# Performance work log

Measured on AMD Instinct MI355X. Metric: run time of the kernel, lower is better.

## Reference

```python
import jax, jax.numpy as jnp
import numpy as np

SEQ, B, IN, H = 1024, 1024, 64, 64

def setup_inputs() -> dict:
    key = jax.random.key(0)
    ks = jax.random.split(key, 6)
    s_in = 1.0 / np.sqrt(IN)
    s_h = 1.0 / np.sqrt(H)
    return {
        "x": jax.random.normal(ks[0], (SEQ, B, IN), dtype=jnp.float32),
        "h": jax.random.normal(ks[1], (1, B, H), dtype=jnp.float32),
        # nn.Linear params: weight (out,in), bias (out,)
        "Wx": jax.random.uniform(ks[2], (H, IN), jnp.float32, -s_in, s_in),
        "bx": jax.random.uniform(ks[3], (H,), jnp.float32, -s_in, s_in),
        "Wh": jax.random.uniform(ks[4], (H, H), jnp.float32, -s_h, s_h),
        "bh": jax.random.uniform(ks[5], (H,), jnp.float32, -s_h, s_h),
    }

def reference(x, h, Wx, bx, Wh, bh):
    act = jnp.tanh  # activation='tanh'
    # Precompute input projection for all timesteps: (S,B,H)
    xp = jnp.einsum('sbi,hi->sbh', x, Wx) + bx
    # lin_h(h).sum(0) with h of shape (1,B,H) == lin_h(h[0])
    h0 = act(jnp.einsum('bj,hj->bh', h[0], Wh) + bh + xp[0])

    def step(h_prev, xt):
        h_new = act(jnp.einsum('bj,hj->bh', h_prev, Wh) + bh + xt)
        return h_new, h_new

    h_last, h_rest = jax.lax.scan(step, h0, xp[1:])
    h_seq = jnp.concatenate([h0[None], h_rest], axis=0)  # (S,B,H)
    return h_seq, h_last
```

## Files before the change

### kernel.cpp

```cpp
#include <hip/hip_runtime.h>
#include <stdint.h>

#define SEQ 1024
#define NB  1024
#define HD  64
#define BH  (NB*HD)
#define ROWS_PER_BLK 8

typedef _Float16 f16x8 __attribute__((ext_vector_type(8)));
typedef float    f32x4 __attribute__((ext_vector_type(4)));

__device__ __forceinline__ int swzb(int s) {
    return (s * 16) ^ (((s >> 3) & 7) << 4);
}
__device__ __forceinline__ uint32_t pkrtz(float a, float b) {
    auto h = __builtin_amdgcn_cvt_pkrtz(a, b);
    return __builtin_bit_cast(uint32_t, h);
}
__device__ __forceinline__ float fast_tanh(float a) {
    float e = __builtin_amdgcn_exp2f(a * 2.8853900817779268f);
    return 1.0f - 2.0f * __builtin_amdgcn_rcpf(e + 1.0f);
}

__global__ __launch_bounds__(256) void rnn_kernel(
    const float* __restrict__ x,  const float* __restrict__ h0,
    const float* __restrict__ Wx, const float* __restrict__ bx,
    const float* __restrict__ Wh, const float* __restrict__ bh,
    float* __restrict__ out)
{
    __shared__ uint32_t lds[2][4][256];

    const int tid  = threadIdx.x;
    const int w    = tid >> 6;
    const int lane = tid & 63;
    const int g    = lane >> 4;
    const int n    = lane & 15;
    const int R0   = blockIdx.x * ROWS_PER_BLK;

    const int pT = tid >> 7;
    const int pr = tid & 127;
    const int pg = pr >> 5;
    const int pn = (pr >> 2) & 7;
    const int pq = pr & 3;
    const int k0 = pT * 32 + pg * 8 + pq * 2;
    const int pdw = (swzb(pg * 16 + pn) >> 2) + pq;
    const float* xprod = x + (size_t)(R0 + pn) * HD + k0;

    const int rdw = swzb(lane) >> 2;

    const int hTw = w >> 1;
    const int hdw = (swzb((2 * (w & 1) + (g >> 1)) * 16 + n) >> 2) + 2 * (g & 1);

    const int jrow = 16 * w + n;
    f16x8 whA[2], wxA[2];
    {
        const float* wr = Wh + (size_t)jrow * HD;
        const float* xr = Wx + (size_t)jrow * HD;
        #pragma unroll
        for (int T = 0; T < 2; ++T) {
            f16x8 aw, ax;
            #pragma unroll
            for (int e = 0; e < 8; ++e) {
                aw[e] = (_Float16)wr[T * 32 + g * 8 + e];
                ax[e] = (_Float16)xr[T * 32 + g * 8 + e];
            }
            whA[T] = aw; wxA[T] = ax;
        }
    }
    f32x4 bias;
    {
        const int j4 = 16 * w + 4 * g;
        #pragma unroll
        for (int r = 0; r < 4; ++r) bias[r] = bh[j4 + r] + bx[j4 + r];
    }

    {
        int4 z = {0, 0, 0, 0};
        ((int4*)lds)[tid]       = z;
        ((int4*)lds)[tid + 256] = z;
    }
    __syncthreads();

    {
        float2 hv = *(const float2*)(h0 + (size_t)(R0 + pn) * HD + k0);
        lds[0][pT][pdw] = pkrtz(hv.x, hv.y);
        float2 xv = *(const float2*)(xprod);
        lds[0][2 + pT][pdw] = pkrtz(xv.x, xv.y);
    }
    float2 r1 = *(const float2*)(xprod + (size_t)1 * BH);
    float2 r2 = *(const float2*)(xprod + (size_t)2 * BH);
    float2 r3 = *(const float2*)(xprod + (size_t)3 * BH);
    float2 r0 = *(const float2*)(xprod + (size_t)4 * BH);
    __syncthreads();

    f16x8 fh0, fh1, fx0, fx1;
    fh0 = __builtin_bit_cast(f16x8, *(const int4*)&lds[0][0][rdw]);
    fh1 = __builtin_bit_cast(f16x8, *(const int4*)&lds[0][1][rdw]);
    fx0 = __builtin_bit_cast(f16x8, *(const int4*)&lds[0][2][rdw]);
    fx1 = __builtin_bit_cast(f16x8, *(const int4*)&lds[0][3][rdw]);

    float* outlast = out + (size_t)SEQ * BH;

    auto STEP = [&](int t, float2& rn) {
        f32x4 acc;
        acc = __builtin_amdgcn_mfma_f32_16x16x32_f16(wxA[0], fx0, bias, 0, 0, 0);
        acc = __builtin_amdgcn_mfma_f32_16x16x32_f16(wxA[1], fx1, acc,  0, 0, 0);
        acc = __builtin_amdgcn_mfma_f32_16x16x32_f16(whA[0], fh0, acc,  0, 0, 0);
        acc = __builtin_amdgcn_mfma_f32_16x16x32_f16(whA[1], fh1, acc,  0, 0, 0);

        const int b2 = (t + 1) & 1;
        if (t < SEQ - 1) {
            lds[b2][2 + pT][pdw] = pkrtz(rn.x, rn.y);
        }
        {
            int tl = t + 5; if (tl > SEQ - 1) tl = SEQ - 1;
            rn = *(const float2*)(xprod + (size_t)tl * BH);
        }

        float hv0 = fast_tanh(acc[0]);
        float hv1 = fast_tanh(acc[1]);
        float hv2 = fast_tanh(acc[2]);
        float hv3 = fast_tanh(acc[3]);

        if (t < SEQ - 1) {
            uint32_t e0 = pkrtz(hv0, hv1);
            uint32_t e1 = pkrtz(hv2, hv3);
            *(int2*)&lds[b2][hTw][hdw] = make_int2((int)e0, (int)e1);
            __syncthreads();
            fh0 = __builtin_bit_cast(f16x8, *(const int4*)&lds[b2][0][rdw]);
            fh1 = __builtin_bit_cast(f16x8, *(const int4*)&lds[b2][1][rdw]);
            fx0 = __builtin_bit_cast(f16x8, *(const int4*)&lds[b2][2][rdw]);
            fx1 = __builtin_bit_cast(f16x8, *(const int4*)&lds[b2][3][rdw]);
        }
        if (n < 8) {
            float4 v = make_float4(hv0, hv1, hv2, hv3);
            float* dst = out + (size_t)t * BH + (size_t)(R0 + n) * HD + 16 * w + 4 * g;
            *(float4*)dst = v;
            if (t == SEQ - 1) {
                *(float4*)(outlast + (size_t)(R0 + n) * HD + 16 * w + 4 * g) = v;
            }
        }
    };

    for (int tb = 0; tb < SEQ; tb += 4) {
        STEP(tb + 0, r1);
        STEP(tb + 1, r2);
        STEP(tb + 2, r3);
        STEP(tb + 3, r0);
    }
}

extern "C" void kernel_launch(void* const* d_in, const int* in_sizes, int n_in,
                              void* d_out, int out_size, void* d_ws, size_t ws_size,
                              hipStream_t stream) {
    const float* x  = (const float*)d_in[0];
    const float* h  = (const float*)d_in[1];
    const float* Wx = (const float*)d_in[2];
    const float* bx = (const float*)d_in[3];
    const float* Wh = (const float*)d_in[4];
    const float* bh = (const float*)d_in[5];
    float* out = (float*)d_out;

    rnn_kernel<<<dim3(NB / ROWS_PER_BLK), dim3(256), 0, stream>>>(x, h, Wx, bx, Wh, bh, out);
}
```

Before: 295.7 us.

## Precompute next-step input projection off the recurrent critical path

The input-projection MFMAs for step t+1 now run during step t, using a 4-deep x ring buffer in LDS, so only two dependent Wh MFMAs remain on the serial chain. Those two are split into independent accumulators and summed, which shortens the MFMA dependency depth. A custom barrier waits only on LDS counters, and the global output store now sits before the barrier. The cost is extra LDS, a vector add, and a prefetch distance lengthened by one step.

```diff
diff --git a/kernel.cpp b/kernel.cpp
--- a/kernel.cpp
+++ b/kernel.cpp
@@ -21,6 +21,11 @@
     float e = __builtin_amdgcn_exp2f(a * 2.8853900817779268f);
     return 1.0f - 2.0f * __builtin_amdgcn_rcpf(e + 1.0f);
 }
+__device__ __forceinline__ void sync_lds() {
+    asm volatile("s_waitcnt lgkmcnt(0)" ::: "memory");
+    __builtin_amdgcn_s_barrier();
+    asm volatile("" ::: "memory");
+}
 
 __global__ __launch_bounds__(256) void rnn_kernel(
     const float* __restrict__ x,  const float* __restrict__ h0,
@@ -28,7 +33,8 @@
     const float* __restrict__ Wh, const float* __restrict__ bh,
     float* __restrict__ out)
 {
-    __shared__ uint32_t lds[2][4][256];
+    __shared__ __align__(16) uint32_t hK[2][2][256];
+    __shared__ __align__(16) uint32_t xK[4][2][256];
 
     const int tid  = threadIdx.x;
     const int w    = tid >> 6;
@@ -76,61 +82,63 @@
 
     {
         int4 z = {0, 0, 0, 0};
-        ((int4*)lds)[tid]       = z;
-        ((int4*)lds)[tid + 256] = z;
+        ((int4*)hK)[tid] = z;
+        ((int4*)xK)[tid] = z;
+        ((int4*)xK)[tid + 256] = z;
     }
-    __syncthreads();
+    sync_lds();
 
     {
         float2 hv = *(const float2*)(h0 + (size_t)(R0 + pn) * HD + k0);
-        lds[0][pT][pdw] = pkrtz(hv.x, hv.y);
-        float2 xv = *(const float2*)(xprod);
-        lds[0][2 + pT][pdw] = pkrtz(xv.x, xv.y);
+        hK[0][pT][pdw] = pkrtz(hv.x, hv.y);
+        float2 x0v = *(const float2*)(xprod);
+        xK[0][pT][pdw] = pkrtz(x0v.x, x0v.y);
+        float2 x1v = *(const float2*)(xprod + (size_t)BH);
+        xK[1][pT][pdw] = pkrtz(x1v.x, x1v.y);
     }
-    float2 r1 = *(const float2*)(xprod + (size_t)1 * BH);
-    float2 r2 = *(const float2*)(xprod + (size_t)2 * BH);
-    float2 r3 = *(const float2*)(xprod + (size_t)3 * BH);
-    float2 r0 = *(const float2*)(xprod + (size_t)4 * BH);
-    __syncthreads();
+    float2 r0 = *(const float2*)(xprod + (size_t)2 * BH);
+    float2 r1 = *(const float2*)(xprod + (size_t)3 * BH);
+    float2 r2 = *(const float2*)(xprod + (size_t)4 * BH);
+    float2 r3 = *(const float2*)(xprod + (size_t)5 * BH);
+    sync_lds();
 
-    f16x8 fh0, fh1, fx0, fx1;
-    fh0 = __builtin_bit_cast(f16x8, *(const int4*)&lds[0][0][rdw]);
-    fh1 = __builtin_bit_cast(f16x8, *(const int4*)&lds[0][1][rdw]);
-    fx0 = __builtin_bit_cast(f16x8, *(const int4*)&lds[0][2][rdw]);
-    fx1 = __builtin_bit_cast(f16x8, *(const int4*)&lds[0][3][rdw]);
-
+    f16x8 fh0 = __builtin_bit_cast(f16x8, *(const int4*)&hK[0][0][rdw]);
+    f16x8 fh1 = __builtin_bit_cast(f16x8, *(const int4*)&hK[0][1][rdw]);
+    const f32x4 zf = {0.f, 0.f, 0.f, 0.f};
+    f32x4 xpA, xpB;
+    {
+        f16x8 fx0 = __builtin_bit_cast(f16x8, *(const int4*)&xK[0][0][rdw]);
+        f16x8 fx1 = __builtin_bit_cast(f16x8, *(const int4*)&xK[0][1][rdw]);
+        xpA = __builtin_amdgcn_mfma_f32_16x16x32_f16(wxA[0], fx0, bias, 0, 0, 0);
+        xpB = __builtin_amdgcn_mfma_f32_16x16x32_f16(wxA[1], fx1, zf,   0, 0, 0);
+    }
     float* outlast = out + (size_t)SEQ * BH;
 
     auto STEP = [&](int t, float2& rn) {
-        f32x4 acc;
-        acc = __builtin_amdgcn_mfma_f32_16x16x32_f16(wxA[0], fx0, bias, 0, 0, 0);
-        acc = __builtin_amdgcn_mfma_f32_16x16x32_f16(wxA[1], fx1, acc,  0, 0, 0);
-        acc = __builtin_amdgcn_mfma_f32_16x16x32_f16(whA[0], fh0, acc,  0, 0, 0);
-        acc = __builtin_amdgcn_mfma_f32_16x16x32_f16(whA[1], fh1, acc,  0, 0, 0);
+        f32x4 accA = __builtin_amdgcn_mfma_f32_16x16x32_f16(whA[0], fh0, xpA, 0, 0, 0);
+        f32x4 accB = __builtin_amdgcn_mfma_f32_16x16x32_f16(whA[1], fh1, xpB, 0, 0, 0);
 
-        const int b2 = (t + 1) & 1;
-        if (t < SEQ - 1) {
-            lds[b2][2 + pT][pdw] = pkrtz(rn.x, rn.y);
-        }
+        if (t + 2 < SEQ) xK[(t + 2) & 3][pT][pdw] = pkrtz(rn.x, rn.y);
         {
-            int tl = t + 5; if (tl > SEQ - 1) tl = SEQ - 1;
+            int tl = t + 6; if (tl > SEQ - 1) tl = SEQ - 1;
             rn = *(const float2*)(xprod + (size_t)tl * BH);
         }
+        if (t + 1 < SEQ) {
+            f16x8 fxn0 = __builtin_bit_cast(f16x8, *(const int4*)&xK[(t + 1) & 3][0][rdw]);
+            f16x8 fxn1 = __builtin_bit_cast(f16x8, *(const int4*)&xK[(t + 1) & 3][1][rdw]);
+            xpA = __builtin_amdgcn_mfma_f32_16x16x32_f16(wxA[0], fxn0, bias, 0, 0, 0);
+            xpB = __builtin_amdgcn_mfma_f32_16x16x32_f16(wxA[1], fxn1, zf,   0, 0, 0);
+        }
 
+        f32x4 acc = accA + accB;
         float hv0 = fast_tanh(acc[0]);
         float hv1 = fast_tanh(acc[1]);
         float hv2 = fast_tanh(acc[2]);
         float hv3 = fast_tanh(acc[3]);
 
-        if (t < SEQ - 1) {
-            uint32_t e0 = pkrtz(hv0, hv1);
-            uint32_t e1 = pkrtz(hv2, hv3);
-            *(int2*)&lds[b2][hTw][hdw] = make_int2((int)e0, (int)e1);
-            __syncthreads();
-            fh0 = __builtin_bit_cast(f16x8, *(const int4*)&lds[b2][0][rdw]);
-            fh1 = __builtin_bit_cast(f16x8, *(const int4*)&lds[b2][1][rdw]);
-            fx0 = __builtin_bit_cast(f16x8, *(const int4*)&lds[b2][2][rdw]);
-            fx1 = __builtin_bit_cast(f16x8, *(const int4*)&lds[b2][3][rdw]);
+        if (t + 1 < SEQ) {
+            *(int2*)&hK[(t + 1) & 1][hTw][hdw] =
+                make_int2((int)pkrtz(hv0, hv1), (int)pkrtz(hv2, hv3));
         }
         if (n < 8) {
             float4 v = make_float4(hv0, hv1, hv2, hv3);
@@ -140,13 +148,18 @@
                 *(float4*)(outlast + (size_t)(R0 + n) * HD + 16 * w + 4 * g) = v;
             }
         }
+        if (t + 1 < SEQ) {
+            sync_lds();
+            fh0 = __builtin_bit_cast(f16x8, *(const int4*)&hK[(t + 1) & 1][0][rdw]);
+            fh1 = __builtin_bit_cast(f16x8, *(const int4*)&hK[(t + 1) & 1][1][rdw]);
+        }
     };
 
     for (int tb = 0; tb < SEQ; tb += 4) {
-        STEP(tb + 0, r1);
-        STEP(tb + 1, r2);
-        STEP(tb + 2, r3);
-        STEP(tb + 3, r0);
+        STEP(tb + 0, r0);
+        STEP(tb + 1, r1);
+        STEP(tb + 2, r2);
+        STEP(tb + 3, r3);
     }
 }
 
```

Result: slower. 308.4 us (+4.3%).

## Run each batch tile in one wavefront using cross-lane permutes instead of LDS barriers

Applied to the files above, without the earlier changes.

Each block now holds all four 16-row output tiles in a single 64-lane wavefront. The recurrent hidden state is redistributed between lanes with permlane32/16 swaps (falling back to ds_bpermute), which removes the per-step LDS write, __syncthreads and LDS reads. The input projection for the next step is computed by MFMA off the critical path, and log2(e)*2 is folded into the weights and bias so tanh needs no multiply. The cost is a 4x larger serial MFMA chain per wave, fewer waves overall, and a runtime probe of permlane semantics to pick the shuffle variant.

```diff
diff --git a/kernel.cpp b/kernel.cpp
--- a/kernel.cpp
+++ b/kernel.cpp
@@ -5,149 +5,232 @@
 #define NB  1024
 #define HD  64
 #define BH  (NB*HD)
-#define ROWS_PER_BLK 8
+#define RPW 8
 
 typedef _Float16 f16x8 __attribute__((ext_vector_type(8)));
 typedef float    f32x4 __attribute__((ext_vector_type(4)));
-
-__device__ __forceinline__ int swzb(int s) {
-    return (s * 16) ^ (((s >> 3) & 7) << 4);
-}
+typedef uint32_t u32x4 __attribute__((ext_vector_type(4)));
+
+#define L2E2 2.8853900817779268f
+
+#if __has_builtin(__builtin_amdgcn_permlane32_swap) && __has_builtin(__builtin_amdgcn_permlane16_swap)
+#define HAVE_PERMLANE 1
+#else
+#define HAVE_PERMLANE 0
+#endif
+
+template<int V> struct IC { static constexpr int value = V; };
+
 __device__ __forceinline__ uint32_t pkrtz(float a, float b) {
     auto h = __builtin_amdgcn_cvt_pkrtz(a, b);
     return __builtin_bit_cast(uint32_t, h);
 }
-__device__ __forceinline__ float fast_tanh(float a) {
-    float e = __builtin_amdgcn_exp2f(a * 2.8853900817779268f);
+__device__ __forceinline__ float tanh_scaled(float a2) {
+    float e = __builtin_amdgcn_exp2f(a2);
     return 1.0f - 2.0f * __builtin_amdgcn_rcpf(e + 1.0f);
 }
 
-__global__ __launch_bounds__(256) void rnn_kernel(
+__global__ __launch_bounds__(64, 1) void rnn_kernel(
     const float* __restrict__ x,  const float* __restrict__ h0,
     const float* __restrict__ Wx, const float* __restrict__ bx,
     const float* __restrict__ Wh, const float* __restrict__ bh,
     float* __restrict__ out)
 {
-    __shared__ uint32_t lds[2][4][256];
-
-    const int tid  = threadIdx.x;
-    const int w    = tid >> 6;
-    const int lane = tid & 63;
+    const int lane = threadIdx.x;
     const int g    = lane >> 4;
     const int n    = lane & 15;
-    const int R0   = blockIdx.x * ROWS_PER_BLK;
-
-    const int pT = tid >> 7;
-    const int pr = tid & 127;
-    const int pg = pr >> 5;
-    const int pn = (pr >> 2) & 7;
-    const int pq = pr & 3;
-    const int k0 = pT * 32 + pg * 8 + pq * 2;
-    const int pdw = (swzb(pg * 16 + pn) >> 2) + pq;
-    const float* xprod = x + (size_t)(R0 + pn) * HD + k0;
-
-    const int rdw = swzb(lane) >> 2;
-
-    const int hTw = w >> 1;
-    const int hdw = (swzb((2 * (w & 1) + (g >> 1)) * 16 + n) >> 2) + 2 * (g & 1);
-
-    const int jrow = 16 * w + n;
-    f16x8 whA[2], wxA[2];
-    {
-        const float* wr = Wh + (size_t)jrow * HD;
-        const float* xr = Wx + (size_t)jrow * HD;
+    const int nc   = n < RPW ? n : RPW - 1;
+    const int R0   = blockIdx.x * RPW;
+    const size_t xoff = (size_t)(R0 + nc) * HD + 8 * g;
+
+    f16x8 whA[4][2], wxA[4][2];
+    #pragma unroll
+    for (int m = 0; m < 4; ++m) {
         #pragma unroll
         for (int T = 0; T < 2; ++T) {
-            f16x8 aw, ax;
+            const float* wr = Wh + (size_t)(16*m + n) * HD + 32*T + 8*g;
+            const float* xr = Wx + (size_t)(16*m + n) * HD + 32*T + 8*g;
+            f32x4 wa = *(const f32x4*)wr, wb = *(const f32x4*)(wr + 4);
+            f32x4 xa = *(const f32x4*)xr, xb = *(const f32x4*)(xr + 4);
+            u32x4 dw, dx;
+            dw[0]=pkrtz(wa[0]*L2E2, wa[1]*L2E2); dw[1]=pkrtz(wa[2]*L2E2, wa[3]*L2E2);
+            dw[2]=pkrtz(wb[0]*L2E2, wb[1]*L2E2); dw[3]=pkrtz(wb[2]*L2E2, wb[3]*L2E2);
+            dx[0]=pkrtz(xa[0]*L2E2, xa[1]*L2E2); dx[1]=pkrtz(xa[2]*L2E2, xa[3]*L2E2);
+            dx[2]=pkrtz(xb[0]*L2E2, xb[1]*L2E2); dx[3]=pkrtz(xb[2]*L2E2, xb[3]*L2E2);
+            whA[m][T] = __builtin_bit_cast(f16x8, dw);
+            wxA[m][T] = __builtin_bit_cast(f16x8, dx);
+        }
+    }
+    f32x4 biasf[4];
+    #pragma unroll
+    for (int m = 0; m < 4; ++m) {
+        f32x4 b1 = *(const f32x4*)(bh + 16*m + 4*g);
+        f32x4 b2 = *(const f32x4*)(bx + 16*m + 4*g);
+        biasf[m] = (b1 + b2) * L2E2;
+    }
+
+    f16x8 fh0, fh1;
+    {
+        const float* hr = h0 + (size_t)(R0 + nc) * HD + 8*g;
+        f32x4 a0 = *(const f32x4*)hr,        a1 = *(const f32x4*)(hr + 4);
+        f32x4 b0 = *(const f32x4*)(hr + 32), b1 = *(const f32x4*)(hr + 36);
+        u32x4 c0, c1;
+        c0[0]=pkrtz(a0[0],a0[1]); c0[1]=pkrtz(a0[2],a0[3]); c0[2]=pkrtz(a1[0],a1[1]); c0[3]=pkrtz(a1[2],a1[3]);
+        c1[0]=pkrtz(b0[0],b0[1]); c1[1]=pkrtz(b0[2],b0[3]); c1[2]=pkrtz(b1[0],b1[1]); c1[3]=pkrtz(b1[2],b1[3]);
+        fh0 = __builtin_bit_cast(f16x8, c0);
+        fh1 = __builtin_bit_cast(f16x8, c1);
+    }
+
+    f32x4 xp[4];
+    {
+        const float* xr = x + xoff;
+        f32x4 a0 = *(const f32x4*)xr,        a1 = *(const f32x4*)(xr + 4);
+        f32x4 b0 = *(const f32x4*)(xr + 32), b1 = *(const f32x4*)(xr + 36);
+        u32x4 c0, c1;
+        c0[0]=pkrtz(a0[0],a0[1]); c0[1]=pkrtz(a0[2],a0[3]); c0[2]=pkrtz(a1[0],a1[1]); c0[3]=pkrtz(a1[2],a1[3]);
+        c1[0]=pkrtz(b0[0],b0[1]); c1[1]=pkrtz(b0[2],b0[3]); c1[2]=pkrtz(b1[0],b1[1]); c1[3]=pkrtz(b1[2],b1[3]);
+        f16x8 fx0 = __builtin_bit_cast(f16x8, c0);
+        f16x8 fx1 = __builtin_bit_cast(f16x8, c1);
+        #pragma unroll
+        for (int m = 0; m < 4; ++m) {
+            f32x4 tq = __builtin_amdgcn_mfma_f32_16x16x32_f16(wxA[m][0], fx0, biasf[m], 0, 0, 0);
+            xp[m]    = __builtin_amdgcn_mfma_f32_16x16x32_f16(wxA[m][1], fx1, tq,       0, 0, 0);
+        }
+    }
+
+    f32x4 ring[4][4];
+    #pragma unroll
+    for (int s = 1; s <= 3; ++s) {
+        const f32x4* xs = (const f32x4*)(x + (size_t)s * BH + xoff);
+        ring[s][0] = xs[0]; ring[s][1] = xs[1]; ring[s][2] = xs[8]; ring[s][3] = xs[9];
+    }
+
+    const int addr0 = ((2*(g&1) + 0) * 16 + n) << 2;
+    const int addr1 = ((2*(g&1) + 1) * 16 + n) << 2;
+
+    auto mainloop = [&](auto mc) {
+        constexpr int  MODE = decltype(mc)::value;
+        constexpr bool PERM = MODE < 4;
+        constexpr bool S1   = (MODE == 2) || (MODE == 3);
+        constexpr bool RF   = (MODE == 1) || (MODE == 3);
+
+        auto cswap32 = [&](uint32_t a, uint32_t b, uint32_t& o0, uint32_t& o1) {
+#if HAVE_PERMLANE
+            auto r = __builtin_amdgcn_permlane32_swap(a, b, false, false);
+            o0 = RF ? (uint32_t)r[1] : (uint32_t)r[0];
+            o1 = RF ? (uint32_t)r[0] : (uint32_t)r[1];
+#else
+            o0 = a; o1 = b;
+#endif
+        };
+        auto cswap16 = [&](uint32_t a, uint32_t b, uint32_t& o0, uint32_t& o1) {
+#if HAVE_PERMLANE
+            auto r = __builtin_amdgcn_permlane16_swap(a, b, false, false);
+            o0 = RF ? (uint32_t)r[1] : (uint32_t)r[0];
+            o1 = RF ? (uint32_t)r[0] : (uint32_t)r[1];
+#else
+            o0 = a; o1 = b;
+#endif
+        };
+
+        for (int tb = 0; tb < SEQ; tb += 4) {
             #pragma unroll
-            for (int e = 0; e < 8; ++e) {
-                aw[e] = (_Float16)wr[T * 32 + g * 8 + e];
-                ax[e] = (_Float16)xr[T * 32 + g * 8 + e];
-            }
-            whA[T] = aw; wxA[T] = ax;
-        }
-    }
-    f32x4 bias;
-    {
-        const int j4 = 16 * w + 4 * g;
-        #pragma unroll
-        for (int r = 0; r < 4; ++r) bias[r] = bh[j4 + r] + bx[j4 + r];
-    }
-
-    {
-        int4 z = {0, 0, 0, 0};
-        ((int4*)lds)[tid]       = z;
-        ((int4*)lds)[tid + 256] = z;
-    }
-    __syncthreads();
-
-    {
-        float2 hv = *(const float2*)(h0 + (size_t)(R0 + pn) * HD + k0);
-        lds[0][pT][pdw] = pkrtz(hv.x, hv.y);
-        float2 xv = *(const float2*)(xprod);
-        lds[0][2 + pT][pdw] = pkrtz(xv.x, xv.y);
-    }
-    float2 r1 = *(const float2*)(xprod + (size_t)1 * BH);
-    float2 r2 = *(const float2*)(xprod + (size_t)2 * BH);
-    float2 r3 = *(const float2*)(xprod + (size_t)3 * BH);
-    float2 r0 = *(const float2*)(xprod + (size_t)4 * BH);
-    __syncthreads();
-
-    f16x8 fh0, fh1, fx0, fx1;
-    fh0 = __builtin_bit_cast(f16x8, *(const int4*)&lds[0][0][rdw]);
-    fh1 = __builtin_bit_cast(f16x8, *(const int4*)&lds[0][1][rdw]);
-    fx0 = __builtin_bit_cast(f16x8, *(const int4*)&lds[0][2][rdw]);
-    fx1 = __builtin_bit_cast(f16x8, *(const int4*)&lds[0][3][rdw]);
-
-    float* outlast = out + (size_t)SEQ * BH;
-
-    auto STEP = [&](int t, float2& rn) {
-        f32x4 acc;
-        acc = __builtin_amdgcn_mfma_f32_16x16x32_f16(wxA[0], fx0, bias, 0, 0, 0);
-        acc = __builtin_amdgcn_mfma_f32_16x16x32_f16(wxA[1], fx1, acc,  0, 0, 0);
-        acc = __builtin_amdgcn_mfma_f32_16x16x32_f16(whA[0], fh0, acc,  0, 0, 0);
-        acc = __builtin_amdgcn_mfma_f32_16x16x32_f16(whA[1], fh1, acc,  0, 0, 0);
-
-        const int b2 = (t + 1) & 1;
-        if (t < SEQ - 1) {
-            lds[b2][2 + pT][pdw] = pkrtz(rn.x, rn.y);
-        }
-        {
-            int tl = t + 5; if (tl > SEQ - 1) tl = SEQ - 1;
-            rn = *(const float2*)(xprod + (size_t)tl * BH);
-        }
-
-        float hv0 = fast_tanh(acc[0]);
-        float hv1 = fast_tanh(acc[1]);
-        float hv2 = fast_tanh(acc[2]);
-        float hv3 = fast_tanh(acc[3]);
-
-        if (t < SEQ - 1) {
-            uint32_t e0 = pkrtz(hv0, hv1);
-            uint32_t e1 = pkrtz(hv2, hv3);
-            *(int2*)&lds[b2][hTw][hdw] = make_int2((int)e0, (int)e1);
-            __syncthreads();
-            fh0 = __builtin_bit_cast(f16x8, *(const int4*)&lds[b2][0][rdw]);
-            fh1 = __builtin_bit_cast(f16x8, *(const int4*)&lds[b2][1][rdw]);
-            fx0 = __builtin_bit_cast(f16x8, *(const int4*)&lds[b2][2][rdw]);
-            fx1 = __builtin_bit_cast(f16x8, *(const int4*)&lds[b2][3][rdw]);
-        }
-        if (n < 8) {
-            float4 v = make_float4(hv0, hv1, hv2, hv3);
-            float* dst = out + (size_t)t * BH + (size_t)(R0 + n) * HD + 16 * w + 4 * g;
-            *(float4*)dst = v;
-            if (t == SEQ - 1) {
-                *(float4*)(outlast + (size_t)(R0 + n) * HD + 16 * w + 4 * g) = v;
+            for (int u = 0; u < 4; ++u) {
+                const int t  = tb + u;
+                const int sc = (u + 1) & 3;
+
+                {
+                    int tl = t + 4; tl = tl > SEQ - 1 ? SEQ - 1 : tl;
+                    const f32x4* xs = (const f32x4*)(x + (size_t)tl * BH + xoff);
+                    ring[u][0] = xs[0]; ring[u][1] = xs[1]; ring[u][2] = xs[8]; ring[u][3] = xs[9];
+                }
+
+                f32x4 acc[4];
+                #pragma unroll
+                for (int m = 0; m < 4; ++m) {
+                    f32x4 hp = __builtin_amdgcn_mfma_f32_16x16x32_f16(whA[m][0], fh0, xp[m], 0, 0, 0);
+                    acc[m]   = __builtin_amdgcn_mfma_f32_16x16x32_f16(whA[m][1], fh1, hp,    0, 0, 0);
+                }
+
+                {
+                    f32x4 r0v = ring[sc][0], r1v = ring[sc][1], r2v = ring[sc][2], r3v = ring[sc][3];
+                    u32x4 c0, c1;
+                    c0[0]=pkrtz(r0v[0],r0v[1]); c0[1]=pkrtz(r0v[2],r0v[3]); c0[2]=pkrtz(r1v[0],r1v[1]); c0[3]=pkrtz(r1v[2],r1v[3]);
+                    c1[0]=pkrtz(r2v[0],r2v[1]); c1[1]=pkrtz(r2v[2],r2v[3]); c1[2]=pkrtz(r3v[0],r3v[1]); c1[3]=pkrtz(r3v[2],r3v[3]);
+                    f16x8 fx0 = __builtin_bit_cast(f16x8, c0);
+                    f16x8 fx1 = __builtin_bit_cast(f16x8, c1);
+                    #pragma unroll
+                    for (int m = 0; m < 4; ++m) {
+                        f32x4 tq = __builtin_amdgcn_mfma_f32_16x16x32_f16(wxA[m][0], fx0, biasf[m], 0, 0, 0);
+                        xp[m]    = __builtin_amdgcn_mfma_f32_16x16x32_f16(wxA[m][1], fx1, tq,       0, 0, 0);
+                    }
+                }
+
+                f32x4 tvv[4]; uint32_t wv[4][2];
+                #pragma unroll
+                for (int m = 0; m < 4; ++m) {
+                    f32x4 a = acc[m], tv;
+                    #pragma unroll
+                    for (int r = 0; r < 4; ++r) tv[r] = tanh_scaled(a[r]);
+                    tvv[m] = tv;
+                    wv[m][0] = pkrtz(tv[0], tv[1]);
+                    wv[m][1] = pkrtz(tv[2], tv[3]);
+                }
+
+                #pragma unroll
+                for (int T = 0; T < 2; ++T) {
+                    u32x4 fd;
+                    if constexpr (PERM) {
+                        #pragma unroll
+                        for (int p = 0; p < 2; ++p) {
+                            uint32_t Ra, Rb, F0, F1;
+                            if constexpr (!S1) cswap32(wv[2*T][p], wv[2*T+1][p], Ra, Rb);
+                            else               cswap32(wv[2*T+1][p], wv[2*T][p], Rb, Ra);
+                            if constexpr (!S1) cswap16(Ra, Rb, F0, F1);
+                            else               cswap16(Rb, Ra, F1, F0);
+                            fd[p]     = F0;
+                            fd[2 + p] = F1;
+                        }
+                    } else {
+                        #pragma unroll
+                        for (int q = 0; q < 4; ++q) {
+                            int ad = (q >> 1) ? addr1 : addr0;
+                            int va = __builtin_amdgcn_ds_bpermute(ad, (int)wv[2*T][q & 1]);
+                            int vb = __builtin_amdgcn_ds_bpermute(ad, (int)wv[2*T+1][q & 1]);
+                            fd[q] = (uint32_t)((g >> 1) ? vb : va);
+                        }
+                    }
+                    if (T == 0) fh0 = __builtin_bit_cast(f16x8, fd);
+                    else        fh1 = __builtin_bit_cast(f16x8, fd);
+                }
+
+                if (n < RPW) {
+                    float* dst = out + (size_t)t * BH + (size_t)(R0 + n) * HD + 4*g;
+                    #pragma unroll
+                    for (int m = 0; m < 4; ++m) *(f32x4*)(dst + 16*m) = tvv[m];
+                    if (t == SEQ - 1) {
+                        float* dl = out + (size_t)SEQ * BH + (size_t)(R0 + n) * HD + 4*g;
+                        #pragma unroll
+                        for (int m = 0; m < 4; ++m) *(f32x4*)(dl + 16*m) = tvv[m];
+                    }
+                }
             }
         }
     };
 
-    for (int tb = 0; tb < SEQ; tb += 4) {
-        STEP(tb + 0, r1);
-        STEP(tb + 1, r2);
-        STEP(tb + 2, r3);
-        STEP(tb + 3, r0);
-    }
+#if HAVE_PERMLANE
+    {
+        auto pr = __builtin_amdgcn_permlane32_swap((uint32_t)lane, (uint32_t)lane + 1000u, false, false);
+        int v = __builtin_amdgcn_readfirstlane((int)pr[0]);
+        if      (v == 0)    mainloop(IC<0>{});
+        else if (v == 32)   mainloop(IC<1>{});
+        else if (v == 1032) mainloop(IC<2>{});
+        else if (v == 1000) mainloop(IC<3>{});
+        else                mainloop(IC<4>{});
+    }
+#else
+    mainloop(IC<4>{});
+#endif
 }
 
 extern "C" void kernel_launch(void* const* d_in, const int* in_sizes, int n_in,
@@ -161,5 +244,5 @@
     const float* bh = (const float*)d_in[5];
     float* out = (float*)d_out;
 
-    rnn_kernel<<<dim3(NB / ROWS_PER_BLK), dim3(256), 0, stream>>>(x, h, Wx, bx, Wh, bh, out);
-}
+    rnn_kernel<<<dim3(NB / RPW), dim3(64), 0, stream>>>(x, h, Wx, bx, Wh, bh, out);
+}
```

After: 436.1 us. +47.5%, slower.
